# Optimization experiments

Measured on AMD Instinct MI355X. Metric: run time of the kernel, lower is better.

The kernel has to match this reference:

```python
import jax, jax.numpy as jnp
import numpy as np

EPS = 1e-5
HEAD_DIM = 2048 // 32  # embed_dim // num_heads -> scale factor only


def _layernorm(x, w):
    # torch: (x - mean) / sqrt(var_biased + eps) * w  (no bias)
    mean = jnp.mean(x, axis=-1, keepdims=True)
    var = jnp.var(x, axis=-1, keepdims=True)  # unbiased=False
    return w * ((x - mean) / jnp.sqrt(var + EPS))


def setup_inputs() -> dict:
    key = jax.random.key(0)
    ks = jax.random.split(key, 9)
    E, F, B, S = 2048, 8192, 2, 4096
    sE = 1.0 / np.sqrt(E)
    sF = 1.0 / np.sqrt(F)
    return {
        "x": jax.random.normal(ks[0], (B, S, E), jnp.float32),
        "ln_w": jnp.ones((E,), jnp.float32),
        "w_q": jax.random.normal(ks[1], (E, E), jnp.float32) * sE,
        "w_k": jax.random.normal(ks[2], (E, E), jnp.float32) * sE,
        "w_v": jax.random.normal(ks[3], (E, E), jnp.float32) * sE,
        "w_o": jax.random.normal(ks[4], (E, E), jnp.float32) * sE,
        "w_gate": jax.random.normal(ks[5], (E, F), jnp.float32) * sE,
        "w_up": jax.random.normal(ks[6], (E, F), jnp.float32) * sE,
        "w_down": jax.random.normal(ks[7], (F, E), jnp.float32) * sF,
    }


def reference(x, ln_w, w_q, w_k, w_v, w_o, w_gate, w_up, w_down):
    # --- pre-attention LN (uses input_layernorm weight) ---
    residual = x
    h = _layernorm(x, ln_w)  # [b, s, e]

    # --- attention exactly as written: transpose(1,2) WITHOUT head split ---
    q = jnp.einsum("bse,ef->bsf", h, w_q).swapaxes(1, 2)  # [b, e, s]
    k = jnp.einsum("bse,ef->bsf", h, w_k).swapaxes(1, 2)  # [b, e, s]
    v = jnp.einsum("bse,ef->bsf", h, w_v).swapaxes(1, 2)  # [b, e, s]
    # scores over the FEATURE axis: [b, e, e]
    scores = jnp.einsum("bes,bfs->bef", q, k) / np.sqrt(HEAD_DIM)
    weights = jax.nn.softmax(scores, axis=-1)
    attn = jnp.einsum("bef,bfs->bes", weights, v)  # [b, e, s]
    attn = attn.swapaxes(1, 2)  # [b, s, e]
    x = jnp.einsum("bse,ef->bsf", attn, w_o) + residual

    # --- pre-MLP LN: the module reuses input_layernorm here (faithful) ---
    residual = x
    h = _layernorm(x, ln_w)

    # --- GELU-gated FFN (exact erf gelu, torch default) ---
    gate = jax.nn.gelu(jnp.einsum("bse,ef->bsf", h, w_gate), approximate=False)
    up = jnp.einsum("bse,ef->bsf", h, w_up)
    out = jnp.einsum("bsf,fe->bse", gate * up, w_down) + residual
    return out
```

## Files before the change

### kernel.cpp

```cpp
#include <hip/hip_runtime.h>
#include <hip/hip_bf16.h>

typedef __hip_bfloat16 bf16;
typedef __attribute__((ext_vector_type(8))) short bf16x8;
typedef __attribute__((ext_vector_type(4))) float f32x4;

#define EPI_BF16 1
#define EPI_BF16_T 2
#define EPI_F32_RES 3
#define EPI_BF16_GELU 4
#define EPI_BF16_MUL 5
#define EPI_F32_KSPLIT 6

__device__ __forceinline__ void gload_lds16(const bf16* g, char* l) {
  __builtin_amdgcn_global_load_lds(
      (const __attribute__((address_space(1))) unsigned int*)g,
      (__attribute__((address_space(3))) unsigned int*)l, 16, 0, 0);
}

#define SCHED0() __builtin_amdgcn_sched_barrier(0)

#define MFQ(Q, AR)                                                                 \
  do {                                                                             \
    __builtin_amdgcn_s_setprio(1);                                                 \
    _Pragma("unroll") for (int j_ = 0; j_ < 2; ++j_)                               \
        _Pragma("unroll") for (int ni_ = 0; ni_ < 4; ++ni_)                        \
            _Pragma("unroll") for (int ks_ = 0; ks_ < 2; ++ks_)                    \
                acc[(Q) * 2 + j_][ni_] = __builtin_amdgcn_mfma_f32_16x16x32_bf16(  \
                    AR[j_][ks_], bfr[ni_][ks_], acc[(Q) * 2 + j_][ni_], 0, 0, 0);  \
    __builtin_amdgcn_s_setprio(0);                                                 \
  } while (0)

template<int EPI>
__global__ __launch_bounds__(512, 2) void gemm256_k(
    const bf16* __restrict__ A, const bf16* __restrict__ B,
    void* __restrict__ Cv, const void* __restrict__ auxv,
    int N, int K, int lda, int ldb,
    long sAz, long sBz, long sCz, int batchM)
{
  __shared__ bf16 lds[4 * 256 * 64];
  char* const As0 = (char*)lds;
  char* const Bs0 = As0 + 32768;
  char* const As1 = Bs0 + 32768;
  char* const Bs1 = As1 + 32768;

  const int gx = gridDim.x, gy = gridDim.y;
  int lid = (blockIdx.z * gy + blockIdx.y) * gx + blockIdx.x;
  const int cpx = (gx * gy * gridDim.z) >> 3;
  lid = (lid & 7) * cpx + (lid >> 3);
  const int bx = lid % gx;
  const int rem = lid / gx;
  const int by = rem % gy;
  const int z = rem / gy;

  int zb = z, part = 0;
  if constexpr (EPI == EPI_F32_KSPLIT) { zb = z & 1; part = z >> 1; }
  A += (size_t)zb * (size_t)sAz + (size_t)part * (size_t)batchM;
  B += (size_t)zb * (size_t)sBz + (size_t)part * (size_t)batchM;

  const int brow = by * 256, bcol = bx * 256;
  const int t = threadIdx.x;
  const int w = t >> 6, lane = t & 63;
  const int wrow = (w >> 2) * 128;
  const int wcol = (w & 3) * 64;
  const int l15 = lane & 15, lg = lane >> 4;

  f32x4 acc[8][4];
#pragma unroll
  for (int i = 0; i < 8; ++i)
#pragma unroll
    for (int j = 0; j < 4; ++j) {
      f32x4 zz = {0.f, 0.f, 0.f, 0.f};
      acc[i][j] = zz;
    }

  auto STAGE = [&](int kk, char* Ad, char* Bd) {
#pragma unroll
    for (int i = 0; i < 4; ++i) {
      const int bslot = (i * 8 + w) * 64;
      const int slot = bslot + lane;
      const int r = slot >> 3;
      const int cs = (slot & 7) ^ (r & 7);
      gload_lds16(A + (size_t)(brow + r) * lda + kk + cs * 8, Ad + bslot * 16);
      gload_lds16(B + (size_t)(bcol + r) * ldb + kk + cs * 8, Bd + bslot * 16);
    }
  };
  auto rdA = [&](const char* Ab, int mi, int ks) {
    const int r = wrow + mi * 16 + l15;
    return *(const bf16x8*)(Ab + ((r * 8 + ((ks * 4 + lg) ^ (r & 7))) << 4));
  };
  auto rdB = [&](const char* Bb, int ni, int ks) {
    const int r = wcol + ni * 16 + l15;
    return *(const bf16x8*)(Bb + ((r * 8 + ((ks * 4 + lg) ^ (r & 7))) << 4));
  };

  STAGE(0, As0, Bs0);
  STAGE(64, As1, Bs1);

  const int NT = K >> 6;
  bf16x8 bfr[4][2], aA[2][2], aB[2][2];

  for (int tt = 0; tt < NT; ++tt) {
    const char* Ar = (tt & 1) ? As1 : As0;
    const char* Br = (tt & 1) ? Bs1 : Bs0;
    char* Aw = (tt & 1) ? As1 : As0;
    char* Bw = (tt & 1) ? Bs1 : Bs0;

    if (tt + 1 < NT) { asm volatile("s_waitcnt vmcnt(8)" ::: "memory"); }
    else             { asm volatile("s_waitcnt vmcnt(0)" ::: "memory"); }
    SCHED0();
    __builtin_amdgcn_s_barrier();
    SCHED0();

    bfr[0][0] = rdB(Br, 0, 0); bfr[0][1] = rdB(Br, 0, 1);
    bfr[1][0] = rdB(Br, 1, 0); bfr[1][1] = rdB(Br, 1, 1);
    bfr[2][0] = rdB(Br, 2, 0); bfr[2][1] = rdB(Br, 2, 1);
    bfr[3][0] = rdB(Br, 3, 0); bfr[3][1] = rdB(Br, 3, 1);
    aA[0][0] = rdA(Ar, 0, 0); aA[0][1] = rdA(Ar, 0, 1);
    aA[1][0] = rdA(Ar, 1, 0); aA[1][1] = rdA(Ar, 1, 1);
    aB[0][0] = rdA(Ar, 2, 0); aB[0][1] = rdA(Ar, 2, 1);
    aB[1][0] = rdA(Ar, 3, 0); aB[1][1] = rdA(Ar, 3, 1);
    MFQ(0, aA);
    aA[0][0] = rdA(Ar, 4, 0); aA[0][1] = rdA(Ar, 4, 1);
    aA[1][0] = rdA(Ar, 5, 0); aA[1][1] = rdA(Ar, 5, 1);
    MFQ(1, aB);
    aB[0][0] = rdA(Ar, 6, 0); aB[0][1] = rdA(Ar, 6, 1);
    aB[1][0] = rdA(Ar, 7, 0); aB[1][1] = rdA(Ar, 7, 1);
    MFQ(2, aA);
    asm volatile("s_waitcnt lgkmcnt(0)" ::: "memory");
    SCHED0();
    __builtin_amdgcn_s_barrier();
    SCHED0();
    if (tt + 2 < NT) STAGE((tt + 2) * 64, Aw, Bw);
    MFQ(3, aB);
  }

  if constexpr (EPI == EPI_BF16_T) {
    bf16* C = (bf16*)Cv + (size_t)zb * (size_t)sCz;
#pragma unroll
    for (int mi = 0; mi < 8; ++mi) {
      const int mbase = brow + wrow + mi * 16 + lg * 4;
      const int bi = mbase / batchM;
      const int ms = mbase - bi * batchM;
      const size_t base = (size_t)bi * (size_t)N * (size_t)batchM + (size_t)ms;
#pragma unroll
      for (int ni = 0; ni < 4; ++ni) {
        const int n = bcol + wcol + ni * 16 + l15;
        union { short4 s; short h[4]; } u;
#pragma unroll
        for (int r = 0; r < 4; ++r) {
          bf16 bv = __float2bfloat16(acc[mi][ni][r]);
          u.h[r] = *(short*)&bv;
        }
        *(short4*)(C + base + (size_t)n * (size_t)batchM) = u.s;
      }
    }
  } else {
#pragma unroll
    for (int mi = 0; mi < 8; ++mi) {
#pragma unroll
      for (int r = 0; r < 4; ++r) {
        const int m = brow + wrow + mi * 16 + lg * 4 + r;
#pragma unroll
        for (int ni = 0; ni < 4; ++ni) {
          const int n = bcol + wcol + ni * 16 + l15;
          const size_t idx = (size_t)m * (size_t)N + (size_t)n;
          float v = acc[mi][ni][r];
          if constexpr (EPI == EPI_F32_KSPLIT) {
            float* C = (part ? (float*)auxv : (float*)Cv) + (size_t)zb * (size_t)sCz;
            C[idx] = v;
          } else if constexpr (EPI == EPI_F32_RES) {
            ((float*)Cv)[idx] = v + ((const float*)auxv)[idx];
          } else if constexpr (EPI == EPI_BF16) {
            ((bf16*)Cv)[idx] = __float2bfloat16(v);
          } else if constexpr (EPI == EPI_BF16_GELU) {
            v = 0.5f * v * (1.0f + erff(v * 0.70710678118654752f));
            ((bf16*)Cv)[idx] = __float2bfloat16(v);
          } else if constexpr (EPI == EPI_BF16_MUL) {
            v = v * __bfloat162float(((const bf16*)auxv)[idx]);
            ((bf16*)Cv)[idx] = __float2bfloat16(v);
          }
        }
      }
    }
  }
}

__global__ __launch_bounds__(256) void ln_k(const float* __restrict__ x,
                                            const float* __restrict__ w,
                                            bf16* __restrict__ out) {
  const int row = blockIdx.x;
  const int t = threadIdx.x;
  const float* xr = x + (size_t)row * 2048;
  float4 a = ((const float4*)xr)[2 * t];
  float4 b = ((const float4*)xr)[2 * t + 1];
  float s = a.x + a.y + a.z + a.w + b.x + b.y + b.z + b.w;
  float ss = a.x * a.x + a.y * a.y + a.z * a.z + a.w * a.w +
             b.x * b.x + b.y * b.y + b.z * b.z + b.w * b.w;
#pragma unroll
  for (int o = 1; o < 64; o <<= 1) { s += __shfl_xor(s, o); ss += __shfl_xor(ss, o); }
  __shared__ float ps[4], pss[4];
  if ((t & 63) == 0) { ps[t >> 6] = s; pss[t >> 6] = ss; }
  __syncthreads();
  s = ps[0] + ps[1] + ps[2] + ps[3];
  ss = pss[0] + pss[1] + pss[2] + pss[3];
  const float mean = s * (1.0f / 2048.0f);
  const float var = ss * (1.0f / 2048.0f) - mean * mean;
  const float rstd = rsqrtf(var + 1e-5f);
  float4 wa = ((const float4*)w)[2 * t];
  float4 wb = ((const float4*)w)[2 * t + 1];
  bf16* o8 = out + (size_t)row * 2048 + (size_t)t * 8;
  o8[0] = __float2bfloat16((a.x - mean) * rstd * wa.x);
  o8[1] = __float2bfloat16((a.y - mean) * rstd * wa.y);
  o8[2] = __float2bfloat16((a.z - mean) * rstd * wa.z);
  o8[3] = __float2bfloat16((a.w - mean) * rstd * wa.w);
  o8[4] = __float2bfloat16((b.x - mean) * rstd * wb.x);
  o8[5] = __float2bfloat16((b.y - mean) * rstd * wb.y);
  o8[6] = __float2bfloat16((b.z - mean) * rstd * wb.z);
  o8[7] = __float2bfloat16((b.w - mean) * rstd * wb.w);
}

__global__ __launch_bounds__(256) void softmax2_k(const float* __restrict__ s0,
                                                  const float* __restrict__ s1,
                                                  bf16* __restrict__ o) {
  const int row = blockIdx.x;
  const int t = threadIdx.x;
  const float* r0 = s0 + (size_t)row * 2048;
  const float* r1 = s1 + (size_t)row * 2048;
  float4 a = ((const float4*)r0)[2 * t];
  float4 b = ((const float4*)r0)[2 * t + 1];
  float4 c = ((const float4*)r1)[2 * t];
  float4 d = ((const float4*)r1)[2 * t + 1];
  float v[8] = {a.x + c.x, a.y + c.y, a.z + c.z, a.w + c.w,
                b.x + d.x, b.y + d.y, b.z + d.z, b.w + d.w};
  float m = -1e30f;
#pragma unroll
  for (int i = 0; i < 8; ++i) { v[i] *= 0.125f; m = fmaxf(m, v[i]); }
#pragma unroll
  for (int o2 = 1; o2 < 64; o2 <<= 1) m = fmaxf(m, __shfl_xor(m, o2));
  __shared__ float red[4];
  if ((t & 63) == 0) red[t >> 6] = m;
  __syncthreads();
  m = fmaxf(fmaxf(red[0], red[1]), fmaxf(red[2], red[3]));
  float sum = 0.f;
#pragma unroll
  for (int i = 0; i < 8; ++i) { v[i] = __expf(v[i] - m); sum += v[i]; }
#pragma unroll
  for (int o2 = 1; o2 < 64; o2 <<= 1) sum += __shfl_xor(sum, o2);
  __syncthreads();
  if ((t & 63) == 0) red[t >> 6] = sum;
  __syncthreads();
  sum = red[0] + red[1] + red[2] + red[3];
  const float inv = 1.0f / sum;
  bf16* po = o + (size_t)row * 2048 + (size_t)t * 8;
#pragma unroll
  for (int i = 0; i < 8; ++i) po[i] = __float2bfloat16(v[i] * inv);
}

__global__ __launch_bounds__(256) void transp_k(const float* __restrict__ in,
                                                bf16* __restrict__ out,
                                                int K, int N) {
  __shared__ float tile[32][33];
  const int bn = blockIdx.x * 32;
  const int bk = blockIdx.y * 32;
  const int tx = threadIdx.x;
  const int ty = threadIdx.y;
#pragma unroll
  for (int i = 0; i < 32; i += 8)
    tile[ty + i][tx] = in[(size_t)(bk + ty + i) * N + bn + tx];
  __syncthreads();
#pragma unroll
  for (int i = 0; i < 32; i += 8)
    out[(size_t)(bn + ty + i) * K + bk + tx] = __float2bfloat16(tile[tx][ty + i]);
}

extern "C" void kernel_launch(void* const* d_in, const int* in_sizes, int n_in,
                              void* d_out, int out_size, void* d_ws, size_t ws_size,
                              hipStream_t stream) {
  (void)in_sizes; (void)n_in; (void)out_size; (void)ws_size;
  const float* x   = (const float*)d_in[0];
  const float* lnw = (const float*)d_in[1];
  const float* w_q = (const float*)d_in[2];
  const float* w_k = (const float*)d_in[3];
  const float* w_v = (const float*)d_in[4];
  const float* w_o = (const float*)d_in[5];
  const float* w_g = (const float*)d_in[6];
  const float* w_u = (const float*)d_in[7];
  const float* w_d = (const float*)d_in[8];
  float* out = (float*)d_out;

  const int E = 2048, F = 8192;
  const size_t MB = 1024ull * 1024ull;
  char* ws = (char*)d_ws;

  bf16* wq_t = (bf16*)(ws + 0 * MB);
  bf16* wk_t = (bf16*)(ws + 8 * MB);
  bf16* wv_t = (bf16*)(ws + 16 * MB);
  bf16* wo_t = (bf16*)(ws + 24 * MB);
  bf16* wg_t = (bf16*)(ws + 32 * MB);
  bf16* wu_t = (bf16*)(ws + 64 * MB);
  bf16* wd_t = (bf16*)(ws + 96 * MB);
  bf16*  h   = (bf16*)(ws + 128 * MB);
  float* sp0 = (float*)(ws + 128 * MB);
  bf16*  h2  = (bf16*)(ws + 128 * MB);
  bf16*  qt    = (bf16*)(ws + 160 * MB);
  bf16*  attnT = (bf16*)(ws + 160 * MB);
  bf16*  gc    = (bf16*)(ws + 160 * MB);
  bf16*  kt  = (bf16*)(ws + 192 * MB);
  bf16*  wts = (bf16*)(ws + 192 * MB);
  bf16*  vm  = (bf16*)(ws + 224 * MB);
  float* x2  = (float*)(ws + 224 * MB);
  float* sp1 = (float*)(ws + 256 * MB);

  dim3 blk(256), tb(32, 8), g512(512);

  transp_k<<<dim3(E / 32, E / 32), tb, 0, stream>>>(w_q, wq_t, E, E);
  transp_k<<<dim3(E / 32, E / 32), tb, 0, stream>>>(w_k, wk_t, E, E);
  transp_k<<<dim3(E / 32, E / 32), tb, 0, stream>>>(w_v, wv_t, E, E);
  transp_k<<<dim3(E / 32, E / 32), tb, 0, stream>>>(w_o, wo_t, E, E);
  transp_k<<<dim3(F / 32, E / 32), tb, 0, stream>>>(w_g, wg_t, E, F);
  transp_k<<<dim3(F / 32, E / 32), tb, 0, stream>>>(w_u, wu_t, E, F);
  transp_k<<<dim3(E / 32, F / 32), tb, 0, stream>>>(w_d, wd_t, F, E);

  ln_k<<<8192, blk, 0, stream>>>(x, lnw, h);

  gemm256_k<EPI_BF16_T><<<dim3(8, 32, 1), g512, 0, stream>>>(h, wq_t, qt, nullptr,
      2048, 2048, 2048, 2048, 0, 0, 0, 4096);
  gemm256_k<EPI_BF16_T><<<dim3(8, 32, 1), g512, 0, stream>>>(h, wk_t, kt, nullptr,
      2048, 2048, 2048, 2048, 0, 0, 0, 4096);
  gemm256_k<EPI_BF16><<<dim3(8, 32, 1), g512, 0, stream>>>(h, wv_t, vm, nullptr,
      2048, 2048, 2048, 2048, 0, 0, 0, 1);

  gemm256_k<EPI_F32_KSPLIT><<<dim3(8, 8, 4), g512, 0, stream>>>(qt, kt, sp0, sp1,
      2048, 2048, 4096, 4096, (long)2048 * 4096, (long)2048 * 4096,
      (long)2048 * 2048, 2048);

  softmax2_k<<<4096, blk, 0, stream>>>(sp0, sp1, wts);

  gemm256_k<EPI_BF16_T><<<dim3(16, 8, 2), g512, 0, stream>>>(wts, vm, attnT, nullptr,
      4096, 2048, 2048, 2048, (long)2048 * 2048, (long)4096 * 2048,
      (long)4096 * 2048, 2048);

  gemm256_k<EPI_F32_RES><<<dim3(8, 32, 1), g512, 0, stream>>>(attnT, wo_t, x2, x,
      2048, 2048, 2048, 2048, 0, 0, 0, 1);

  ln_k<<<8192, blk, 0, stream>>>(x2, lnw, h2);

  for (int c = 0; c < 2; ++c) {
    gemm256_k<EPI_BF16_GELU><<<dim3(16, 32, 1), g512, 0, stream>>>(
        h2, wg_t + (size_t)c * 4096 * 2048, gc, nullptr,
        4096, 2048, 2048, 2048, 0, 0, 0, 1);
    gemm256_k<EPI_BF16_MUL><<<dim3(16, 32, 1), g512, 0, stream>>>(
        h2, wu_t + (size_t)c * 4096 * 2048, gc, gc,
        4096, 2048, 2048, 2048, 0, 0, 0, 1);
    gemm256_k<EPI_F32_RES><<<dim3(8, 32, 1), g512, 0, stream>>>(
        gc, wd_t + (size_t)c * 4096, out,
        (c == 0 ? (const void*)x2 : (const void*)out),
        2048, 4096, 4096, 8192, 0, 0, 0, 1);
  }
}
```

Baseline: 1.426 ms.

## Restructure GEMM main loop into 2x2 quadrant MFMA schedule with interleaved LDS reads

Reorganizes the 256x256 GEMM inner loop so each wave computes four M-by-N quadrants (4 A fragments by 2 B fragments) instead of four M-row groups over all B fragments. LDS fragment reads are split into smaller batches interleaved with barriers and MFMA bursts, and the global-load wait plus barrier for the next tile is moved to the end of the iteration. The intent is to overlap LDS reads with MFMA work and reduce register pressure from holding all B fragments. It adds more barriers per iteration, which may cost synchronization overhead.

```diff
diff --git a/kernel.cpp b/kernel.cpp
--- a/kernel.cpp
+++ b/kernel.cpp
@@ -20,15 +20,17 @@
 
 #define SCHED0() __builtin_amdgcn_sched_barrier(0)
 
-#define MFQ(Q, AR)                                                                 \
-  do {                                                                             \
-    __builtin_amdgcn_s_setprio(1);                                                 \
-    _Pragma("unroll") for (int j_ = 0; j_ < 2; ++j_)                               \
-        _Pragma("unroll") for (int ni_ = 0; ni_ < 4; ++ni_)                        \
-            _Pragma("unroll") for (int ks_ = 0; ks_ < 2; ++ks_)                    \
-                acc[(Q) * 2 + j_][ni_] = __builtin_amdgcn_mfma_f32_16x16x32_bf16(  \
-                    AR[j_][ks_], bfr[ni_][ks_], acc[(Q) * 2 + j_][ni_], 0, 0, 0);  \
-    __builtin_amdgcn_s_setprio(0);                                                 \
+#define MFQ(MB, NB)                                                               \
+  do {                                                                            \
+    __builtin_amdgcn_s_setprio(1);                                                \
+    _Pragma("unroll") for (int mi_ = 0; mi_ < 4; ++mi_)                           \
+        _Pragma("unroll") for (int nj_ = 0; nj_ < 2; ++nj_)                       \
+            _Pragma("unroll") for (int ks_ = 0; ks_ < 2; ++ks_)                   \
+                acc[(MB) * 4 + mi_][(NB) * 2 + nj_] =                             \
+                    __builtin_amdgcn_mfma_f32_16x16x32_bf16(                      \
+                        aR[mi_][ks_], bR[(NB) * 2 + nj_][ks_],                    \
+                        acc[(MB) * 4 + mi_][(NB) * 2 + nj_], 0, 0, 0);            \
+    __builtin_amdgcn_s_setprio(0);                                                \
   } while (0)
 
 template<int EPI>
@@ -96,43 +98,62 @@
 
   STAGE(0, As0, Bs0);
   STAGE(64, As1, Bs1);
+  asm volatile("s_waitcnt vmcnt(8)" ::: "memory");
+  SCHED0();
+  __builtin_amdgcn_s_barrier();
 
   const int NT = K >> 6;
-  bf16x8 bfr[4][2], aA[2][2], aB[2][2];
-
-  for (int tt = 0; tt < NT; ++tt) {
-    const char* Ar = (tt & 1) ? As1 : As0;
-    const char* Br = (tt & 1) ? Bs1 : Bs0;
-    char* Aw = (tt & 1) ? As1 : As0;
-    char* Bw = (tt & 1) ? Bs1 : Bs0;
-
-    if (tt + 1 < NT) { asm volatile("s_waitcnt vmcnt(8)" ::: "memory"); }
-    else             { asm volatile("s_waitcnt vmcnt(0)" ::: "memory"); }
+  bf16x8 aR[4][2], bR[4][2];
+
+  for (int v = 0; v < NT; ++v) {
+    const char* Ab = (v & 1) ? As1 : As0;
+    const char* Bb = (v & 1) ? Bs1 : Bs0;
+    char* Aw = (v & 1) ? As1 : As0;
+    char* Bw = (v & 1) ? Bs1 : Bs0;
+
+#pragma unroll
+    for (int mi_ = 0; mi_ < 4; ++mi_) {
+      aR[mi_][0] = rdA(Ab, mi_, 0); aR[mi_][1] = rdA(Ab, mi_, 1);
+    }
+    bR[0][0] = rdB(Bb, 0, 0); bR[0][1] = rdB(Bb, 0, 1);
+    bR[1][0] = rdB(Bb, 1, 0); bR[1][1] = rdB(Bb, 1, 1);
+    asm volatile("s_waitcnt lgkmcnt(8)" ::: "memory");
     SCHED0();
     __builtin_amdgcn_s_barrier();
-    SCHED0();
-
-    bfr[0][0] = rdB(Br, 0, 0); bfr[0][1] = rdB(Br, 0, 1);
-    bfr[1][0] = rdB(Br, 1, 0); bfr[1][1] = rdB(Br, 1, 1);
-    bfr[2][0] = rdB(Br, 2, 0); bfr[2][1] = rdB(Br, 2, 1);
-    bfr[3][0] = rdB(Br, 3, 0); bfr[3][1] = rdB(Br, 3, 1);
-    aA[0][0] = rdA(Ar, 0, 0); aA[0][1] = rdA(Ar, 0, 1);
-    aA[1][0] = rdA(Ar, 1, 0); aA[1][1] = rdA(Ar, 1, 1);
-    aB[0][0] = rdA(Ar, 2, 0); aB[0][1] = rdA(Ar, 2, 1);
-    aB[1][0] = rdA(Ar, 3, 0); aB[1][1] = rdA(Ar, 3, 1);
-    MFQ(0, aA);
-    aA[0][0] = rdA(Ar, 4, 0); aA[0][1] = rdA(Ar, 4, 1);
-    aA[1][0] = rdA(Ar, 5, 0); aA[1][1] = rdA(Ar, 5, 1);
-    MFQ(1, aB);
-    aB[0][0] = rdA(Ar, 6, 0); aB[0][1] = rdA(Ar, 6, 1);
-    aB[1][0] = rdA(Ar, 7, 0); aB[1][1] = rdA(Ar, 7, 1);
-    MFQ(2, aA);
     asm volatile("s_waitcnt lgkmcnt(0)" ::: "memory");
     SCHED0();
-    __builtin_amdgcn_s_barrier();
+    MFQ(0, 0);
+    __builtin_amdgcn_s_barrier();
+
+    bR[2][0] = rdB(Bb, 2, 0); bR[2][1] = rdB(Bb, 2, 1);
+    bR[3][0] = rdB(Bb, 3, 0); bR[3][1] = rdB(Bb, 3, 1);
+    __builtin_amdgcn_s_barrier();
+    asm volatile("s_waitcnt lgkmcnt(0)" ::: "memory");
     SCHED0();
-    if (tt + 2 < NT) STAGE((tt + 2) * 64, Aw, Bw);
-    MFQ(3, aB);
+    MFQ(0, 1);
+    __builtin_amdgcn_s_barrier();
+
+#pragma unroll
+    for (int mi_ = 0; mi_ < 4; ++mi_) {
+      aR[mi_][0] = rdA(Ab, 4 + mi_, 0); aR[mi_][1] = rdA(Ab, 4 + mi_, 1);
+    }
+    __builtin_amdgcn_s_barrier();
+    asm volatile("s_waitcnt lgkmcnt(0)" ::: "memory");
+    SCHED0();
+    MFQ(1, 0);
+    __builtin_amdgcn_s_barrier();
+
+    if (v + 2 < NT) STAGE((v + 2) * 64, Aw, Bw);
+    MFQ(1, 1);
+    if (v + 2 < NT) {
+      asm volatile("s_waitcnt vmcnt(8)" ::: "memory");
+      SCHED0();
+      __builtin_amdgcn_s_barrier();
+    } else if (v + 1 < NT) {
+      asm volatile("s_waitcnt vmcnt(0)" ::: "memory");
+      SCHED0();
+      __builtin_amdgcn_s_barrier();
+    }
   }
 
   if constexpr (EPI == EPI_BF16_T) {
```

New measurement: 1.471 ms. 1.03x slower.

## Restructure GEMM main loop into half-K stages with finer-grained LDS pipelining

Applied to the files above, without the earlier changes.

The 256x256 bf16 GEMM main loop is reorganised to stage 32-wide K halves into four LDS slots instead of two 64-wide buffers. Loads for the next half-tile are issued in a rotating schedule with explicit vmcnt and barrier points. LDS reads now go through inline-asm ds_read_b128 with immediate offsets and a new 4-chunk XOR swizzle. The MFMA issue order also changes to 4x4 blocks per half. The aim is finer overlap of global-to-LDS copies with MFMA work and lower address arithmetic, at the cost of many more barriers per K tile and hand-tuned waitcnt logic that could be fragile.

```diff
diff --git a/kernel.cpp b/kernel.cpp
--- a/kernel.cpp
+++ b/kernel.cpp
@@ -18,17 +18,48 @@
       (__attribute__((address_space(3))) unsigned int*)l, 16, 0, 0);
 }
 
+__device__ __forceinline__ unsigned lds_addr(const void* p) {
+  return (unsigned)(size_t)(const __attribute__((address_space(3))) char*)p;
+}
+
+template<int IMM>
+__device__ __forceinline__ bf16x8 dsr(unsigned addr) {
+  bf16x8 d;
+  asm volatile("ds_read_b128 %0, %1 offset:%c2" : "=v"(d) : "v"(addr), "i"(IMM));
+  return d;
+}
+
 #define SCHED0() __builtin_amdgcn_sched_barrier(0)
-
-#define MFQ(Q, AR)                                                                 \
-  do {                                                                             \
-    __builtin_amdgcn_s_setprio(1);                                                 \
-    _Pragma("unroll") for (int j_ = 0; j_ < 2; ++j_)                               \
-        _Pragma("unroll") for (int ni_ = 0; ni_ < 4; ++ni_)                        \
-            _Pragma("unroll") for (int ks_ = 0; ks_ < 2; ++ks_)                    \
-                acc[(Q) * 2 + j_][ni_] = __builtin_amdgcn_mfma_f32_16x16x32_bf16(  \
-                    AR[j_][ks_], bfr[ni_][ks_], acc[(Q) * 2 + j_][ni_], 0, 0, 0);  \
-    __builtin_amdgcn_s_setprio(0);                                                 \
+#define VMG(N) asm volatile("s_waitcnt vmcnt(" #N ")" ::: "memory")
+#define BAR_LGKM()                                   \
+  do {                                               \
+    __builtin_amdgcn_s_barrier();                    \
+    asm volatile("s_waitcnt lgkmcnt(0)" ::: "memory"); \
+    SCHED0();                                        \
+  } while (0)
+
+#define RDX(BUF)                                                            \
+  do {                                                                      \
+    aR[0] = dsr<(BUF) + 0>(aAddr);    aR[1] = dsr<(BUF) + 1024>(aAddr);     \
+    aR[2] = dsr<(BUF) + 2048>(aAddr); aR[3] = dsr<(BUF) + 3072>(aAddr);     \
+    bR[0] = dsr<(BUF) + 0>(bAddr);    bR[1] = dsr<(BUF) + 1024>(bAddr);     \
+    bR[2] = dsr<(BUF) + 2048>(bAddr); bR[3] = dsr<(BUF) + 3072>(bAddr);     \
+  } while (0)
+#define RDY(BUF)                                                            \
+  do {                                                                      \
+    aR[0] = dsr<(BUF) + 4096>(aAddr); aR[1] = dsr<(BUF) + 5120>(aAddr);     \
+    aR[2] = dsr<(BUF) + 6144>(aAddr); aR[3] = dsr<(BUF) + 7168>(aAddr);     \
+  } while (0)
+
+#define MFQH(MB)                                                            \
+  do {                                                                      \
+    __builtin_amdgcn_s_setprio(1);                                          \
+    _Pragma("unroll") for (int mi_ = 0; mi_ < 4; ++mi_)                     \
+        _Pragma("unroll") for (int nj_ = 0; nj_ < 4; ++nj_)                 \
+            acc[(MB) * 4 + mi_][nj_] =                                      \
+                __builtin_amdgcn_mfma_f32_16x16x32_bf16(                    \
+                    aR[mi_], bR[nj_], acc[(MB) * 4 + mi_][nj_], 0, 0, 0);   \
+    __builtin_amdgcn_s_setprio(0);                                          \
   } while (0)
 
 template<int EPI>
@@ -38,11 +69,7 @@
     int N, int K, int lda, int ldb,
     long sAz, long sBz, long sCz, int batchM)
 {
-  __shared__ bf16 lds[4 * 256 * 64];
-  char* const As0 = (char*)lds;
-  char* const Bs0 = As0 + 32768;
-  char* const As1 = Bs0 + 32768;
-  char* const Bs1 = As1 + 32768;
+  __shared__ bf16 lds[2 * 4 * 16384 / 2];
 
   const int gx = gridDim.x, gy = gridDim.y;
   int lid = (blockIdx.z * gy + blockIdx.y) * gx + blockIdx.x;
@@ -74,65 +101,73 @@
       acc[i][j] = zz;
     }
 
-  auto STAGE = [&](int kk, char* Ad, char* Bd) {
-#pragma unroll
-    for (int i = 0; i < 4; ++i) {
-      const int bslot = (i * 8 + w) * 64;
+  auto STAGE1 = [&](int tile, int kh) {
+    const int par = tile & 1;
+    char* Ad = (char*)lds + (((par << 1) | kh) << 14);
+    char* Bd = Ad + 65536;
+    const int kk = tile * 64 + kh * 32;
+    const int csw = (lane >> 3) & 3;
+#pragma unroll
+    for (int j = 0; j < 2; ++j) {
+      const int bslot = (j * 8 + w) * 64;
       const int slot = bslot + lane;
-      const int r = slot >> 3;
-      const int cs = (slot & 7) ^ (r & 7);
+      const int r = slot >> 2;
+      const int cs = (slot & 3) ^ csw;
       gload_lds16(A + (size_t)(brow + r) * lda + kk + cs * 8, Ad + bslot * 16);
       gload_lds16(B + (size_t)(bcol + r) * ldb + kk + cs * 8, Bd + bslot * 16);
     }
   };
-  auto rdA = [&](const char* Ab, int mi, int ks) {
-    const int r = wrow + mi * 16 + l15;
-    return *(const bf16x8*)(Ab + ((r * 8 + ((ks * 4 + lg) ^ (r & 7))) << 4));
-  };
-  auto rdB = [&](const char* Bb, int ni, int ks) {
-    const int r = wcol + ni * 16 + l15;
-    return *(const bf16x8*)(Bb + ((r * 8 + ((ks * 4 + lg) ^ (r & 7))) << 4));
-  };
-
-  STAGE(0, As0, Bs0);
-  STAGE(64, As1, Bs1);
+
+  const unsigned chm = (unsigned)((lg ^ ((l15 >> 1) & 3)) * 16);
+  const unsigned aAddr = lds_addr(lds) + (unsigned)((wrow + l15) * 64) + chm;
+  const unsigned bAddr = lds_addr(lds) + 65536u + (unsigned)((wcol + l15) * 64) + chm;
+
+  STAGE1(0, 0);
+  STAGE1(0, 1);
+  STAGE1(1, 0);
+  VMG(8);
+  SCHED0();
+  __builtin_amdgcn_s_barrier();
 
   const int NT = K >> 6;
-  bf16x8 bfr[4][2], aA[2][2], aB[2][2];
-
-  for (int tt = 0; tt < NT; ++tt) {
-    const char* Ar = (tt & 1) ? As1 : As0;
-    const char* Br = (tt & 1) ? Bs1 : Bs0;
-    char* Aw = (tt & 1) ? As1 : As0;
-    char* Bw = (tt & 1) ? Bs1 : Bs0;
-
-    if (tt + 1 < NT) { asm volatile("s_waitcnt vmcnt(8)" ::: "memory"); }
-    else             { asm volatile("s_waitcnt vmcnt(0)" ::: "memory"); }
-    SCHED0();
-    __builtin_amdgcn_s_barrier();
-    SCHED0();
-
-    bfr[0][0] = rdB(Br, 0, 0); bfr[0][1] = rdB(Br, 0, 1);
-    bfr[1][0] = rdB(Br, 1, 0); bfr[1][1] = rdB(Br, 1, 1);
-    bfr[2][0] = rdB(Br, 2, 0); bfr[2][1] = rdB(Br, 2, 1);
-    bfr[3][0] = rdB(Br, 3, 0); bfr[3][1] = rdB(Br, 3, 1);
-    aA[0][0] = rdA(Ar, 0, 0); aA[0][1] = rdA(Ar, 0, 1);
-    aA[1][0] = rdA(Ar, 1, 0); aA[1][1] = rdA(Ar, 1, 1);
-    aB[0][0] = rdA(Ar, 2, 0); aB[0][1] = rdA(Ar, 2, 1);
-    aB[1][0] = rdA(Ar, 3, 0); aB[1][1] = rdA(Ar, 3, 1);
-    MFQ(0, aA);
-    aA[0][0] = rdA(Ar, 4, 0); aA[0][1] = rdA(Ar, 4, 1);
-    aA[1][0] = rdA(Ar, 5, 0); aA[1][1] = rdA(Ar, 5, 1);
-    MFQ(1, aB);
-    aB[0][0] = rdA(Ar, 6, 0); aB[0][1] = rdA(Ar, 6, 1);
-    aB[1][0] = rdA(Ar, 7, 0); aB[1][1] = rdA(Ar, 7, 1);
-    MFQ(2, aA);
-    asm volatile("s_waitcnt lgkmcnt(0)" ::: "memory");
-    SCHED0();
-    __builtin_amdgcn_s_barrier();
-    SCHED0();
-    if (tt + 2 < NT) STAGE((tt + 2) * 64, Aw, Bw);
-    MFQ(3, aB);
+  bf16x8 aR[4], bR[4];
+
+  for (int t2 = 0; t2 < NT; t2 += 2) {
+    const bool s3 = (t2 + 2) < NT;
+    const bool s7 = (t2 + 3) < NT;
+
+    RDX(0);
+    STAGE1(t2 + 1, 1);
+    BAR_LGKM(); MFQH(0);
+    __builtin_amdgcn_s_barrier();
+    RDY(0);
+    BAR_LGKM(); MFQH(1);
+    VMG(8);
+    __builtin_amdgcn_s_barrier();
+    RDX(16384);
+    if (s3) STAGE1(t2 + 2, 0);
+    BAR_LGKM(); MFQH(0);
+    __builtin_amdgcn_s_barrier();
+    RDY(16384);
+    BAR_LGKM(); MFQH(1);
+    if (s3) VMG(8); else VMG(4);
+    __builtin_amdgcn_s_barrier();
+    RDX(32768);
+    if (s3) STAGE1(t2 + 2, 1);
+    BAR_LGKM(); MFQH(0);
+    __builtin_amdgcn_s_barrier();
+    RDY(32768);
+    BAR_LGKM(); MFQH(1);
+    if (s3) VMG(8); else VMG(0);
+    __builtin_amdgcn_s_barrier();
+    RDX(49152);
+    if (s7) STAGE1(t2 + 3, 0);
+    BAR_LGKM(); MFQH(0);
+    __builtin_amdgcn_s_barrier();
+    RDY(49152);
+    BAR_LGKM(); MFQH(1);
+    if (s3) { if (s7) VMG(8); else VMG(4); }
+    __builtin_amdgcn_s_barrier();
   }
 
   if constexpr (EPI == EPI_BF16_T) {
```

Result: slower. 1.484 ms (+4.1%).
